# Kernel optimization log

Hardware: AMD Instinct MI355X
Metric: run time of the kernel (lower is better)

Reference implementation:

```python
import jax, jax.numpy as jnp
import numpy as np

K = 20
EPS = 1e-5

def setup_inputs() -> dict:
    key = jax.random.key(0)
    ks = jax.random.split(key, 12)
    B, C, N, O, E = 8, 64, 4096, 64, 128
    x = jax.random.normal(ks[0], (B, C, N), dtype=jnp.float32)
    domain_emb = jax.random.normal(ks[1], (B, E), dtype=jnp.float32)
    s = 0.05
    conv_w = jax.random.normal(ks[2], (O, 2 * C), dtype=jnp.float32) * s  # Conv2d(2C,O,1) weight squeezed
    gw1 = jax.random.normal(ks[3], (E, E), dtype=jnp.float32) * s
    gb1 = jax.random.normal(ks[4], (E,), dtype=jnp.float32) * s
    gw2 = jax.random.normal(ks[5], (O, E), dtype=jnp.float32) * s
    gb2 = jax.random.normal(ks[6], (O,), dtype=jnp.float32) * s
    bw1 = jax.random.normal(ks[7], (E, E), dtype=jnp.float32) * s
    bb1 = jax.random.normal(ks[8], (E,), dtype=jnp.float32) * s
    bw2 = jax.random.normal(ks[9], (O, E), dtype=jnp.float32) * s
    bb2 = jax.random.normal(ks[10], (O,), dtype=jnp.float32) * s
    return {"x": x, "domain_emb": domain_emb, "conv_w": conv_w,
            "gw1": gw1, "gb1": gb1, "gw2": gw2, "gb2": gb2,
            "bw1": bw1, "bb1": bb1, "bw2": bw2, "bb2": bb2}

def _knn_idx(x):
    # x: (B, C, N) -> neighbor indices (B, N, K), self excluded (knn runs on detached x)
    pts = jnp.transpose(jax.lax.stop_gradient(x), (0, 2, 1))  # (B, N, C)
    sq = jnp.sum(pts * pts, axis=-1)  # (B, N)
    # squared Euclidean distance; same topk ordering as torch.cdist
    d2 = sq[:, :, None] + sq[:, None, :] - 2.0 * jnp.einsum('bnc,bmc->bnm', pts, pts)
    _, idx = jax.lax.top_k(-d2, K + 1)  # smallest K+1 distances
    return idx[:, :, 1:]  # drop self

def _mlp(e, w1, b1, w2, b2):
    h = jax.nn.relu(e @ w1.T + b1)
    return h @ w2.T + b2

def reference(x, domain_emb, conv_w, gw1, gb1, gw2, gb2, bw1, bb1, bw2, bb2):
    B, C, N = x.shape
    idx = _knn_idx(x)                              # (B, N, K)
    pts = jnp.transpose(x, (0, 2, 1))              # (B, N, C), differentiable
    bidx = jnp.arange(B)[:, None, None]
    nbr = pts[bidx, idx]                           # (B, N, K, C)
    ctr = pts[:, :, None, :]                       # (B, N, 1, C)
    # edge feature: concat(neighbor - center, center) -> (B, N, K, 2C)
    feat = jnp.concatenate([nbr - ctr, jnp.broadcast_to(ctr, nbr.shape)], axis=-1)
    # 1x1 conv == per-edge linear; then max over neighbors
    out = jnp.einsum('bnkc,oc->bonk', feat, conv_w)  # (B, O, N, K)
    out = jnp.max(out, axis=-1)                      # (B, O, N)
    # InstanceNorm1d (affine=False): per (b, channel) stats over N
    mean = jnp.mean(out, axis=-1, keepdims=True)
    var = jnp.mean((out - mean) ** 2, axis=-1, keepdims=True)
    xn = (out - mean) / jnp.sqrt(var + EPS)
    gamma = 1.0 + _mlp(domain_emb, gw1, gb1, gw2, gb2)[:, :, None]  # (B, O, 1)
    beta = _mlp(domain_emb, bw1, bb1, bw2, bb2)[:, :, None]
    return jax.nn.relu(xn * gamma + beta)
```

## Files before the change

kernel.cpp:

```cpp
#include <hip/hip_runtime.h>

#define B_ 8
#define C_ 64
#define N_ 4096
#define O_ 64
#define E_ 128
#define K_ 20
#define EPS_ 1e-5f

typedef float v2f __attribute__((ext_vector_type(2)));
typedef __attribute__((ext_vector_type(4)))  int  i32x4;
typedef __attribute__((ext_vector_type(16))) int  i32x16;
typedef __attribute__((ext_vector_type(16))) char c16;

#define WS_SQ    0
#define WS_Y     32768
#define WS_Z     (WS_Y + B_*N_*O_)
#define WS_M     (WS_Z + B_*N_*O_)
#define WS_GAMMA (WS_M + B_*N_*O_)
#define WS_BETA  (WS_GAMMA + 512)
#define WS_SCALE (WS_BETA + 512)
#define WS_SHIFT (WS_SCALE + 512)
#define WS_END_F (WS_SHIFT + 512)
#define WS_I8B   (WS_END_F * 4)

__global__ __launch_bounds__(256) void k0_mlp(const float* __restrict__ emb,
    const float* __restrict__ gw1, const float* __restrict__ gb1,
    const float* __restrict__ gw2, const float* __restrict__ gb2,
    const float* __restrict__ bw1, const float* __restrict__ bb1,
    const float* __restrict__ bw2, const float* __restrict__ bb2,
    float* __restrict__ ws)
{
  __shared__ float s_emb[B_][E_];
  __shared__ float s_h[2][B_][E_];
  int t = threadIdx.x;
  for (int i = t; i < B_*E_; i += 256) s_emb[i >> 7][i & 127] = emb[i];
  __syncthreads();
  {
    int net = t >> 7, e = t & 127;
    const float* w1 = net ? bw1 : gw1;
    const float* b1 = net ? bb1 : gb1;
    float acc[B_];
#pragma unroll
    for (int b = 0; b < B_; ++b) acc[b] = 0.f;
    const float* row = w1 + e * E_;
    for (int j = 0; j < E_; j += 4) {
      float4 w = *(const float4*)(row + j);
#pragma unroll
      for (int b = 0; b < B_; ++b)
        acc[b] += s_emb[b][j]*w.x + s_emb[b][j+1]*w.y + s_emb[b][j+2]*w.z + s_emb[b][j+3]*w.w;
    }
    float bias = b1[e];
#pragma unroll
    for (int b = 0; b < B_; ++b) s_h[net][b][e] = fmaxf(acc[b] + bias, 0.f);
  }
  __syncthreads();
  for (int r = 0; r < 4; ++r) {
    int idx = t + 256 * r;
    int net = idx >> 9, b = (idx >> 6) & 7, o = idx & 63;
    const float* w2 = net ? bw2 : gw2;
    const float* b2 = net ? bb2 : gb2;
    const float* row = w2 + o * E_;
    float acc = 0.f;
    for (int e = 0; e < E_; e += 4) {
      float4 w = *(const float4*)(row + e);
      acc += s_h[net][b][e]*w.x + s_h[net][b][e+1]*w.y + s_h[net][b][e+2]*w.z + s_h[net][b][e+3]*w.w;
    }
    acc += b2[o];
    if (net == 0) ws[WS_GAMMA + b*O_ + o] = 1.f + acc;
    else          ws[WS_BETA  + b*O_ + o] = acc;
  }
}

__global__ __launch_bounds__(256) void k1a_split(const float* __restrict__ x, float* __restrict__ ws)
{
  __shared__ double sqp[4][64];
  int b = blockIdx.y, T = blockIdx.x, n0 = T * 64;
  int t = threadIdx.x;
  int r = t & 63, qc = t >> 6;
  char* blob = (char*)ws + WS_I8B + (size_t)(b * 64 + T) * 16384;
  c16 v0, v1, v2;
  double sq = 0.0;
#pragma unroll
  for (int e = 0; e < 16; ++e) {
    int c = qc * 16 + e;
    float v = x[((size_t)(b * 64 + c)) * 4096 + n0 + r];
    int X = __float2int_rn(v * 1048576.0f);
    sq += (double)X * (double)X;
    int L0 = ((X + 128) & 255) - 128;
    int X1 = (X - L0) >> 8;
    int L1 = ((X1 + 128) & 255) - 128;
    int L2 = (X1 - L1) >> 8;
    v0[e] = (char)L0; v1[e] = (char)L1; v2[e] = (char)L2;
  }
  *(c16*)(blob + 0*5120 + r*80 + qc*16) = v0;
  *(c16*)(blob + 1*5120 + r*80 + qc*16) = v1;
  *(c16*)(blob + 2*5120 + r*80 + qc*16) = v2;
  sqp[qc][r] = sq;
  __syncthreads();
  if (t < 64)
    ws[WS_SQ + b * N_ + n0 + t] =
      (float)((sqp[0][t] + sqp[1][t] + sqp[2][t] + sqp[3][t]) * (1.0 / 1099511627776.0));
}

__global__ __launch_bounds__(256) void k1b_yz(const float* __restrict__ x,
                                              const float* __restrict__ cw_, float* __restrict__ ws)
{
  extern __shared__ char l1b[];
  float* P   = (float*)l1b;
  float* waT = (float*)(l1b + 16640);
  float* wbT = (float*)(l1b + 33024);
  float* YT  = (float*)l1b;
  float* ZT  = (float*)(l1b + 16900);
  int b = blockIdx.y, n0 = blockIdx.x * 64;
  int t = threadIdx.x;
  {
    int o = t & 63, cb = t >> 6;
#pragma unroll
    for (int k = 0; k < 16; ++k) {
      int c = cb + 4 * k;
      float w1v = cw_[o * 128 + c];
      float w2v = cw_[o * 128 + 64 + c];
      waT[c * 64 + o] = w1v;
      wbT[c * 64 + o] = w2v - w1v;
    }
  }
  {
    int nl = t & 63, cw4 = t >> 6;
#pragma unroll
    for (int k = 0; k < 16; ++k) {
      int c = cw4 + 4 * k;
      P[nl * 65 + c] = x[((size_t)b * C_ + c) * N_ + n0 + nl];
    }
  }
  __syncthreads();
  int n = t & 63, og = t >> 6;
  v2f accY[8], accZ[8];
  const v2f zero2 = {0.f, 0.f};
#pragma unroll
  for (int i = 0; i < 8; ++i) { accY[i] = zero2; accZ[i] = zero2; }
  for (int c = 0; c < C_; ++c) {
    float p = P[n * 65 + c];
    v2f pp = {p, p};
    const v2f* wa2 = (const v2f*)&waT[c * 64 + og * 16];
    const v2f* wb2 = (const v2f*)&wbT[c * 64 + og * 16];
#pragma unroll
    for (int i = 0; i < 8; ++i) {
      accY[i] = __builtin_elementwise_fma(pp, wa2[i], accY[i]);
      accZ[i] = __builtin_elementwise_fma(pp, wb2[i], accZ[i]);
    }
  }
  __syncthreads();
#pragma unroll
  for (int i = 0; i < 8; ++i) {
    YT[n * 65 + og * 16 + 2 * i + 0] = accY[i][0];
    YT[n * 65 + og * 16 + 2 * i + 1] = accY[i][1];
    ZT[n * 65 + og * 16 + 2 * i + 0] = accZ[i][0];
    ZT[n * 65 + og * 16 + 2 * i + 1] = accZ[i][1];
  }
  __syncthreads();
  {
    int nr = t >> 2, o0 = (t & 3) * 16;
    size_t gbase = ((size_t)b * N_ + n0 + nr) * O_ + o0;
#pragma unroll
    for (int j = 0; j < 16; j += 4) {
      float4 yv, zv;
      yv.x = YT[nr * 65 + o0 + j + 0]; yv.y = YT[nr * 65 + o0 + j + 1];
      yv.z = YT[nr * 65 + o0 + j + 2]; yv.w = YT[nr * 65 + o0 + j + 3];
      zv.x = ZT[nr * 65 + o0 + j + 0]; zv.y = ZT[nr * 65 + o0 + j + 1];
      zv.z = ZT[nr * 65 + o0 + j + 2]; zv.w = ZT[nr * 65 + o0 + j + 3];
      *(float4*)&ws[WS_Y + gbase + j] = yv;
      *(float4*)&ws[WS_Z + gbase + j] = zv;
    }
  }
}
#define K1B_LDS 49408

#define K2_LDS 66560

struct FragT {
  i32x4 a00, a01, a10, a11, a20, a21;
  float4 s0, s1, s2, s3;
};

__global__ __launch_bounds__(256, 2) void k2_knn(float* __restrict__ ws)
{
  extern __shared__ char lds_raw[];
  float2* list2 = (float2*)lds_raw;
  float2* lmrg  = (float2*)(lds_raw + 40960);
  int*    fidx  = (int*)(lds_raw + 61440);
  float*  Mt    = (float*)lds_raw;

  const int t = threadIdx.x;
  const int bid = blockIdx.x;
  const int b = bid & 7;
  const int n0 = (bid >> 3) * 64;
  const int w = t >> 6, l = t & 63, lo5 = l & 31, hi = l >> 5;
  const int qloc = (w & 1) * 32 + lo5;
  const int qg = n0 + qloc;
  const int mhalf = (w >> 1) * 32;
  const int rowm = mhalf + lo5;

  const char* __restrict__ i8b = (const char*)ws + WS_I8B + (size_t)b * 64 * 16384;
  const float* __restrict__ sqg = ws + WS_SQ + (size_t)b * N_;

  i32x4 Bq00, Bq01, Bq10, Bq11, Bq20, Bq21;
  {
    const char* qb = i8b + (size_t)(n0 >> 6) * 16384 + qloc * 80 + hi * 16;
    Bq00 = *(const i32x4*)(qb + 0);      Bq01 = *(const i32x4*)(qb + 32);
    Bq10 = *(const i32x4*)(qb + 5120);   Bq11 = *(const i32x4*)(qb + 5152);
    Bq20 = *(const i32x4*)(qb + 10240);  Bq21 = *(const i32x4*)(qb + 10272);
  }

  float kd[K_]; int ki[K_];
#pragma unroll
  for (int i = 0; i < K_; ++i) { kd[i] = __builtin_inff(); ki[i] = 0; }
  float kd19 = __builtin_inff();

  auto LOADF = [&](FragT& F, int tile) {
    const char* bb = i8b + (size_t)tile * 16384 + rowm * 80 + hi * 16;
    F.a00 = *(const i32x4*)(bb + 0);      F.a01 = *(const i32x4*)(bb + 32);
    F.a10 = *(const i32x4*)(bb + 5120);   F.a11 = *(const i32x4*)(bb + 5152);
    F.a20 = *(const i32x4*)(bb + 10240);  F.a21 = *(const i32x4*)(bb + 10272);
    const float* sp = sqg + tile * 64 + mhalf + 4 * hi;
    F.s0 = *(const float4*)(sp + 0);  F.s1 = *(const float4*)(sp + 8);
    F.s2 = *(const float4*)(sp + 16); F.s3 = *(const float4*)(sp + 24);
  };

  auto BODY = [&](const FragT& F, int step) {
    i32x16 accA = {0,0,0,0,0,0,0,0,0,0,0,0,0,0,0,0};
    i32x16 accB = {0,0,0,0,0,0,0,0,0,0,0,0,0,0,0,0};
    i32x16 accC = {0,0,0,0,0,0,0,0,0,0,0,0,0,0,0,0};
    i32x16 accD = {0,0,0,0,0,0,0,0,0,0,0,0,0,0,0,0};
    accA = __builtin_amdgcn_mfma_i32_32x32x32_i8(F.a20, Bq20, accA, 0, 0, 0);
    accB = __builtin_amdgcn_mfma_i32_32x32x32_i8(F.a20, Bq10, accB, 0, 0, 0);
    accC = __builtin_amdgcn_mfma_i32_32x32x32_i8(F.a10, Bq10, accC, 0, 0, 0);
    accD = __builtin_amdgcn_mfma_i32_32x32x32_i8(F.a10, Bq00, accD, 0, 0, 0);
    accA = __builtin_amdgcn_mfma_i32_32x32x32_i8(F.a21, Bq21, accA, 0, 0, 0);
    accB = __builtin_amdgcn_mfma_i32_32x32x32_i8(F.a10, Bq20, accB, 0, 0, 0);
    accC = __builtin_amdgcn_mfma_i32_32x32x32_i8(F.a20, Bq00, accC, 0, 0, 0);
    accD = __builtin_amdgcn_mfma_i32_32x32x32_i8(F.a00, Bq10, accD, 0, 0, 0);
    accB = __builtin_amdgcn_mfma_i32_32x32x32_i8(F.a21, Bq11, accB, 0, 0, 0);
    accC = __builtin_amdgcn_mfma_i32_32x32x32_i8(F.a00, Bq20, accC, 0, 0, 0);
    accD = __builtin_amdgcn_mfma_i32_32x32x32_i8(F.a11, Bq01, accD, 0, 0, 0);
    accB = __builtin_amdgcn_mfma_i32_32x32x32_i8(F.a11, Bq21, accB, 0, 0, 0);
    accC = __builtin_amdgcn_mfma_i32_32x32x32_i8(F.a11, Bq11, accC, 0, 0, 0);
    accD = __builtin_amdgcn_mfma_i32_32x32x32_i8(F.a01, Bq11, accD, 0, 0, 0);
    accC = __builtin_amdgcn_mfma_i32_32x32x32_i8(F.a21, Bq01, accC, 0, 0, 0);
    accC = __builtin_amdgcn_mfma_i32_32x32x32_i8(F.a01, Bq21, accC, 0, 0, 0);

    float sqa[16] = { F.s0.x,F.s0.y,F.s0.z,F.s0.w, F.s1.x,F.s1.y,F.s1.z,F.s1.w,
                      F.s2.x,F.s2.y,F.s2.z,F.s2.w, F.s3.x,F.s3.y,F.s3.z,F.s3.w };
    const int mbase = step * 64 + mhalf + 4 * hi;
#pragma unroll
    for (int r = 0; r < 16; ++r) {
      float key = fmaf((float)accD[r], -4.656612873077393e-10f,
                  fmaf((float)accC[r], -1.1920928955078125e-7f,
                  fmaf((float)accB[r], -3.0517578125e-5f,
                  fmaf((float)accA[r], -0.0078125f, sqa[r]))));
      int m = mbase + (r & 3) + 8 * (r >> 2);
      bool want = (key < kd19) & (m != qg);
      if (__any(want)) {
        if (want) {
          bool cc[K_];
#pragma unroll
          for (int i = 0; i < K_; ++i) cc[i] = key < kd[i];
#pragma unroll
          for (int i = K_ - 1; i >= 1; --i) {
            kd[i] = cc[i-1] ? kd[i-1] : (cc[i] ? key : kd[i]);
            ki[i] = cc[i-1] ? ki[i-1] : (cc[i] ? m : ki[i]);
          }
          kd[0] = cc[0] ? key : kd[0];
          ki[0] = cc[0] ? m : ki[0];
        }
        kd19 = kd[K_ - 1];
      }
    }
  };

  FragT FA, FB;
  LOADF(FA, 0);
#pragma unroll 1
  for (int s = 0; s < 64; s += 2) {
    LOADF(FB, s + 1);
    BODY(FA, s);
    LOADF(FA, (s + 2 < 64) ? (s + 2) : 63);
    BODY(FB, s + 1);
  }

  {
    int j = (w >> 1) * 2 + hi;
#pragma unroll
    for (int s = 0; s < K_; ++s)
      list2[(size_t)(qloc * 4 + j) * K_ + s] = make_float2(kd[s], __int_as_float(ki[s]));
  }
  __syncthreads();
  if (t < 128) {
    int q = t & 63, h = t >> 6;
    const float2* la = &list2[(size_t)(q * 4 + 2 * h) * K_];
    const float2* lb = &list2[(size_t)(q * 4 + 2 * h + 1) * K_];
    float2* lo = &lmrg[(size_t)(q * 2 + h) * K_];
    int ia = 0, ib2 = 0;
#pragma unroll 1
    for (int k = 0; k < K_; ++k) {
      float2 fa = la[ia];
      float2 fb = lb[ib2];
      bool ta = fa.x <= fb.x;
      lo[k] = ta ? fa : fb;
      ia += ta ? 1 : 0; ib2 += ta ? 0 : 1;
    }
  }
  __syncthreads();
  if (t < 64) {
    const float2* la = &lmrg[(size_t)(t * 2) * K_];
    const float2* lb = &lmrg[(size_t)(t * 2 + 1) * K_];
    int ia = 0, ib2 = 0;
#pragma unroll 1
    for (int k = 0; k < K_; ++k) {
      float2 fa = la[ia];
      float2 fb = lb[ib2];
      bool ta = fa.x <= fb.x;
      fidx[t * K_ + k] = __float_as_int(ta ? fa.y : fb.y);
      ia += ta ? 1 : 0; ib2 += ta ? 0 : 1;
    }
  }
  __syncthreads();
  {
    int q = t & 63;
    int ob = (t >> 6) * 16;
    const float* __restrict__ Yb = ws + WS_Y + (size_t)b * N_ * O_;
    float4 mx[4];
#pragma unroll
    for (int i = 0; i < 4; ++i)
      mx[i] = make_float4(-__builtin_inff(), -__builtin_inff(), -__builtin_inff(), -__builtin_inff());
#pragma unroll 1
    for (int k = 0; k < K_; ++k) {
      int m = fidx[q * K_ + k];
      const float4* yr = (const float4*)&Yb[(size_t)m * O_ + ob];
#pragma unroll
      for (int i = 0; i < 4; ++i) {
        float4 v = yr[i];
        mx[i].x = fmaxf(mx[i].x, v.x);
        mx[i].y = fmaxf(mx[i].y, v.y);
        mx[i].z = fmaxf(mx[i].z, v.z);
        mx[i].w = fmaxf(mx[i].w, v.w);
      }
    }
    const float4* zr = (const float4*)&ws[WS_Z + ((size_t)b * N_ + n0 + q) * O_ + ob];
#pragma unroll
    for (int i = 0; i < 4; ++i) {
      float4 z = zr[i];
      Mt[q * 69 + ob + 4 * i + 0] = mx[i].x + z.x;
      Mt[q * 69 + ob + 4 * i + 1] = mx[i].y + z.y;
      Mt[q * 69 + ob + 4 * i + 2] = mx[i].z + z.z;
      Mt[q * 69 + ob + 4 * i + 3] = mx[i].w + z.w;
    }
  }
  __syncthreads();
  {
    int o = t >> 2, seg = (t & 3) * 16;
    float* Mrow = ws + WS_M + ((size_t)b * O_ + o) * N_ + n0 + seg;
#pragma unroll
    for (int i = 0; i < 16; i += 4) {
      float4 wv;
      wv.x = Mt[(seg + i + 0) * 69 + o];
      wv.y = Mt[(seg + i + 1) * 69 + o];
      wv.z = Mt[(seg + i + 2) * 69 + o];
      wv.w = Mt[(seg + i + 3) * 69 + o];
      *(float4*)&Mrow[i] = wv;
    }
  }
}

__global__ __launch_bounds__(256) void k3_stats(float* __restrict__ ws)
{
  int bo = blockIdx.x;
  int t = threadIdx.x;
  const float4* Mr = (const float4*)&ws[WS_M + (size_t)bo * N_];
  float s = 0.f, ss = 0.f;
#pragma unroll
  for (int k = 0; k < 4; ++k) {
    float4 v = Mr[t + 256 * k];
    s  += v.x + v.y + v.z + v.w;
    ss += v.x * v.x + v.y * v.y + v.z * v.z + v.w * v.w;
  }
#pragma unroll
  for (int off = 32; off >= 1; off >>= 1) {
    s  += __shfl_down(s, off);
    ss += __shfl_down(ss, off);
  }
  __shared__ float red[8];
  int w = t >> 6;
  if ((t & 63) == 0) { red[w * 2] = s; red[w * 2 + 1] = ss; }
  __syncthreads();
  if (t == 0) {
    float S  = red[0] + red[2] + red[4] + red[6];
    float SS = red[1] + red[3] + red[5] + red[7];
    float mean = S / (float)N_;
    float var = fmaxf(SS / (float)N_ - mean * mean, 0.f);
    float g  = ws[WS_GAMMA + bo];
    float be = ws[WS_BETA + bo];
    float sc = g / sqrtf(var + EPS_);
    ws[WS_SCALE + bo] = sc;
    ws[WS_SHIFT + bo] = be - mean * sc;
  }
}

__global__ __launch_bounds__(256) void k4_apply(const float* __restrict__ ws, float* __restrict__ out)
{
  int i4 = blockIdx.x * 256 + threadIdx.x;
  int bo = i4 >> 10;
  float sc = ws[WS_SCALE + bo], sh = ws[WS_SHIFT + bo];
  float4 v = *(const float4*)&ws[WS_M + (size_t)i4 * 4];
  float4 r;
  r.x = fmaxf(fmaf(v.x, sc, sh), 0.f);
  r.y = fmaxf(fmaf(v.y, sc, sh), 0.f);
  r.z = fmaxf(fmaf(v.z, sc, sh), 0.f);
  r.w = fmaxf(fmaf(v.w, sc, sh), 0.f);
  *(float4*)&out[(size_t)i4 * 4] = r;
}

extern "C" void kernel_launch(void* const* d_in, const int* in_sizes, int n_in,
                              void* d_out, int out_size, void* d_ws, size_t ws_size,
                              hipStream_t stream)
{
  const float* x   = (const float*)d_in[0];
  const float* emb = (const float*)d_in[1];
  const float* cw  = (const float*)d_in[2];
  const float* gw1 = (const float*)d_in[3];
  const float* gb1 = (const float*)d_in[4];
  const float* gw2 = (const float*)d_in[5];
  const float* gb2 = (const float*)d_in[6];
  const float* bw1 = (const float*)d_in[7];
  const float* bb1 = (const float*)d_in[8];
  const float* bw2 = (const float*)d_in[9];
  const float* bb2 = (const float*)d_in[10];
  float* ws  = (float*)d_ws;
  float* out = (float*)d_out;

  k0_mlp<<<1, 256, 0, stream>>>(emb, gw1, gb1, gw2, gb2, bw1, bb1, bw2, bb2, ws);
  k1a_split<<<dim3(64, 8), 256, 0, stream>>>(x, ws);
  k1b_yz<<<dim3(64, 8), 256, K1B_LDS, stream>>>(x, cw, ws);
  k2_knn<<<512, 256, K2_LDS, stream>>>(ws);
  k3_stats<<<512, 256, 0, stream>>>(ws);
  k4_apply<<<2048, 256, 0, stream>>>(ws, out);
}
```

Measured before the change: 508.2 us.

## Buffer kNN candidates in LDS and batch insertions to cut divergence

Candidate keys that beat the current threshold are no longer inserted into the register top-K list immediately. They are appended to a per-thread pending buffer in LDS and flushed in batches once any lane reaches four pending entries, which should reduce how often a divergent 20-step insertion runs. The two-stage pairwise merge of partial lists is replaced by a single 4-way merge, LDS use is reduced, and launch bounds are raised to 3 blocks per CU. The trade-offs are a stale threshold between flushes, which lets extra candidates through, plus added LDS traffic and register pressure from the higher occupancy target.

```diff
diff --git a/kernel.cpp b/kernel.cpp
--- a/kernel.cpp
+++ b/kernel.cpp
@@ -176,19 +176,20 @@
 }
 #define K1B_LDS 49408
 
-#define K2_LDS 66560
+#define K2_LDS 46080
 
 struct FragT {
   i32x4 a00, a01, a10, a11, a20, a21;
   float4 s0, s1, s2, s3;
 };
 
-__global__ __launch_bounds__(256, 2) void k2_knn(float* __restrict__ ws)
+__global__ __launch_bounds__(256, 3) void k2_knn(float* __restrict__ ws)
 {
   extern __shared__ char lds_raw[];
+  float*  pendk = (float*)lds_raw;
+  int*    pendi = (int*)(lds_raw + 8192);
   float2* list2 = (float2*)lds_raw;
-  float2* lmrg  = (float2*)(lds_raw + 40960);
-  int*    fidx  = (int*)(lds_raw + 61440);
+  int*    fidx  = (int*)(lds_raw + 40960);
   float*  Mt    = (float*)lds_raw;
 
   const int t = threadIdx.x;
@@ -216,6 +217,32 @@
 #pragma unroll
   for (int i = 0; i < K_; ++i) { kd[i] = __builtin_inff(); ki[i] = 0; }
   float kd19 = __builtin_inff();
+  int cnt = 0;
+
+  auto flush = [&]() {
+#pragma unroll 1
+    for (int s = 0; s < 8; ++s) {
+      if (__all(s >= cnt)) break;
+      if (s < cnt) {
+        float kx = pendk[s * 256 + t];
+        int mx = pendi[s * 256 + t];
+        if (kx < kd[K_ - 1]) {
+          bool cc[K_];
+#pragma unroll
+          for (int i = 0; i < K_; ++i) cc[i] = kx < kd[i];
+#pragma unroll
+          for (int i = K_ - 1; i >= 1; --i) {
+            kd[i] = cc[i-1] ? kd[i-1] : (cc[i] ? kx : kd[i]);
+            ki[i] = cc[i-1] ? ki[i-1] : (cc[i] ? mx : ki[i]);
+          }
+          kd[0] = cc[0] ? kx : kd[0];
+          ki[0] = cc[0] ? mx : ki[0];
+        }
+      }
+    }
+    cnt = 0;
+    kd19 = kd[K_ - 1];
+  };
 
   auto LOADF = [&](FragT& F, int tile) {
     const char* bb = i8b + (size_t)tile * 16384 + rowm * 80 + hi * 16;
@@ -259,22 +286,12 @@
                   fmaf((float)accB[r], -3.0517578125e-5f,
                   fmaf((float)accA[r], -0.0078125f, sqa[r]))));
       int m = mbase + (r & 3) + 8 * (r >> 2);
-      bool want = (key < kd19) & (m != qg);
-      if (__any(want)) {
-        if (want) {
-          bool cc[K_];
-#pragma unroll
-          for (int i = 0; i < K_; ++i) cc[i] = key < kd[i];
-#pragma unroll
-          for (int i = K_ - 1; i >= 1; --i) {
-            kd[i] = cc[i-1] ? kd[i-1] : (cc[i] ? key : kd[i]);
-            ki[i] = cc[i-1] ? ki[i-1] : (cc[i] ? m : ki[i]);
-          }
-          kd[0] = cc[0] ? key : kd[0];
-          ki[0] = cc[0] ? m : ki[0];
-        }
-        kd19 = kd[K_ - 1];
+      if ((key < kd19) & (m != qg)) {
+        pendk[cnt * 256 + t] = key;
+        pendi[cnt * 256 + t] = m;
+        ++cnt;
       }
+      if ((r & 3) == 3) { if (__any(cnt >= 4)) flush(); }
     }
   };
 
@@ -287,6 +304,8 @@
     LOADF(FA, (s + 2 < 64) ? (s + 2) : 63);
     BODY(FB, s + 1);
   }
+  flush();
+  __syncthreads();
 
   {
     int j = (w >> 1) * 2 + hi;
@@ -295,33 +314,26 @@
       list2[(size_t)(qloc * 4 + j) * K_ + s] = make_float2(kd[s], __int_as_float(ki[s]));
   }
   __syncthreads();
-  if (t < 128) {
-    int q = t & 63, h = t >> 6;
-    const float2* la = &list2[(size_t)(q * 4 + 2 * h) * K_];
-    const float2* lb = &list2[(size_t)(q * 4 + 2 * h + 1) * K_];
-    float2* lo = &lmrg[(size_t)(q * 2 + h) * K_];
-    int ia = 0, ib2 = 0;
+  if (t < 64) {
+    const float2* la = &list2[(size_t)(t * 4 + 0) * K_];
+    const float2* lb = &list2[(size_t)(t * 4 + 1) * K_];
+    const float2* lc = &list2[(size_t)(t * 4 + 2) * K_];
+    const float2* ld = &list2[(size_t)(t * 4 + 3) * K_];
+    int ia = 0, ib2 = 0, ic = 0, id2 = 0;
 #pragma unroll 1
     for (int k = 0; k < K_; ++k) {
-      float2 fa = la[ia];
-      float2 fb = lb[ib2];
-      bool ta = fa.x <= fb.x;
-      lo[k] = ta ? fa : fb;
-      ia += ta ? 1 : 0; ib2 += ta ? 0 : 1;
-    }
-  }
-  __syncthreads();
-  if (t < 64) {
-    const float2* la = &lmrg[(size_t)(t * 2) * K_];
-    const float2* lb = &lmrg[(size_t)(t * 2 + 1) * K_];
-    int ia = 0, ib2 = 0;
-#pragma unroll 1
-    for (int k = 0; k < K_; ++k) {
-      float2 fa = la[ia];
-      float2 fb = lb[ib2];
-      bool ta = fa.x <= fb.x;
-      fidx[t * K_ + k] = __float_as_int(ta ? fa.y : fb.y);
-      ia += ta ? 1 : 0; ib2 += ta ? 0 : 1;
+      float2 fa = la[ia], fb = lb[ib2], fc = lc[ic], fd = ld[id2];
+      bool tab = fa.x <= fb.x;
+      float2 m1 = tab ? fa : fb;
+      bool tcd = fc.x <= fd.x;
+      float2 m2 = tcd ? fc : fd;
+      bool t12 = m1.x <= m2.x;
+      float2 mm = t12 ? m1 : m2;
+      fidx[t * K_ + k] = __float_as_int(mm.y);
+      ia  += ( tab &  t12) ? 1 : 0;
+      ib2 += (!tab &  t12) ? 1 : 0;
+      ic  += ( tcd & !t12) ? 1 : 0;
+      id2 += (!tcd & !t12) ? 1 : 0;
     }
   }
   __syncthreads();
```

New measurement: 862.6 us. 1.7x slower.
